# Kernel optimization log

Hardware: AMD Instinct MI355X
Metric: run time of the kernel (lower is better)

The kernel has to match this reference:

```python
import jax, jax.numpy as jnp
import numpy as np

N_NODES = 3000
N_FEAT = 2
N_UNITS = 64
BATCH = 16
K_DIFF = 2  # max_diffusion_step


def _supports(adj):
    # dual_random_walk: (D^-1 A)^T and (D'^-1 A^T)^T, rows with zero degree -> 0
    def rw_T(A):
        d = A.sum(axis=1)
        d_inv = jnp.where(d > 0, 1.0 / d, 0.0)
        return (d_inv[:, None] * A).T  # (N, N)
    return [rw_T(adj), rw_T(adj.T)]


def _gconv(inputs, state, supports, W, b, num_nodes):
    # inputs: (B, N*F), state: (B, N*U)
    B = inputs.shape[0]
    x = jnp.concatenate([inputs.reshape(B, num_nodes, -1),
                         state.reshape(B, num_nodes, -1)], axis=2)  # (B, N, C)
    x0 = x.transpose(1, 2, 0)  # (N, C, B)
    mats = [x0]
    for S in supports:
        x1 = jnp.einsum('mn,ncb->mcb', S, x0)
        mats.append(x1)
        xk_1, xk_2 = x1, x0
        for _ in range(2, K_DIFF + 1):
            x2 = 2.0 * jnp.einsum('mn,ncb->mcb', S, xk_1) - xk_2  # Chebyshev recurrence
            mats.append(x2)
            xk_1, xk_2 = x2, xk_1
    xs = jnp.stack(mats, axis=0)  # (M, N, C, B)
    M, _, C, _ = xs.shape
    xs = xs.transpose(3, 1, 2, 0).reshape(B * num_nodes, C * M)
    out = xs @ W + b  # (B*N, O)
    return out.reshape(B, num_nodes * W.shape[1])


def setup_inputs() -> dict:
    key = jax.random.key(0)
    k1, k2, k3, k4, k5 = jax.random.split(key, 5)
    C = N_FEAT + N_UNITS          # 66
    M = 2 * K_DIFF + 1            # 5 (two supports)
    xw = lambda k, s: jax.random.normal(k, s, dtype=jnp.float32) * jnp.sqrt(2.0 / (s[0] + s[1]))
    return {
        "inputs": jax.random.normal(k1, (BATCH, N_NODES * N_FEAT), dtype=jnp.float32),
        "hx": jax.random.normal(k2, (BATCH, N_NODES * N_UNITS), dtype=jnp.float32),
        "adj_mx": jax.random.uniform(k3, (N_NODES, N_NODES), dtype=jnp.float32),
        "W_gate": xw(k4, (C * M, 2 * N_UNITS)),
        "b_gate": jnp.ones((2 * N_UNITS,), dtype=jnp.float32),  # bias_start=1.0
        "W_cand": xw(k5, (C * M, N_UNITS)),
        "b_cand": jnp.zeros((N_UNITS,), dtype=jnp.float32),
        "num_nodes": N_NODES,
    }


def reference(inputs, hx, adj_mx, W_gate, b_gate, W_cand, b_cand, num_nodes):
    supports = _supports(adj_mx)
    B = inputs.shape[0]
    value = jax.nn.sigmoid(_gconv(inputs, hx, supports, W_gate, b_gate, num_nodes))
    value = value.reshape(B, num_nodes, 2 * N_UNITS)
    r, u = value[..., :N_UNITS], value[..., N_UNITS:]
    r = r.reshape(B, num_nodes * N_UNITS)
    u = u.reshape(B, num_nodes * N_UNITS)
    c = jnp.tanh(_gconv(inputs, r * hx, supports, W_cand, b_cand, num_nodes))
    new_state = u * hx + (1.0 - u) * c
    return new_state
```

## Files before the change

kernel.cpp:

```cpp
#include <hip/hip_runtime.h>
#include <cstdint>
#include <cstddef>


typedef unsigned short u16;
typedef __bf16 bf16x8 __attribute__((ext_vector_type(8)));
typedef u16 u16x8 __attribute__((ext_vector_type(8)));
typedef float f32x4 __attribute__((ext_vector_type(4)));

#define NND 3000
#define KP  3008
#define NBX 16
#define NCB 1056
#define NCBP 1152
#define KW  330
#define KWP 352

__device__ __forceinline__ float b2f(u16 x) { return (float)__builtin_bit_cast(__bf16, x); }
__device__ __forceinline__ u16 f2b(float f) { return __builtin_bit_cast(u16, (__bf16)f); }

__device__ __forceinline__ void gll16(const u16* g, void* l) {
  __builtin_amdgcn_global_load_lds(
      (const __attribute__((address_space(1))) unsigned int*)g,
      (__attribute__((address_space(3))) unsigned int*)l, 16, 0, 0);
}


__global__ void k_probe(const u16* __restrict__ bg, int* __restrict__ flag) {
  if (threadIdx.x == 0 && blockIdx.x == 0) *flag = (bg[0] == 0x3F80) ? 0 : 1;
}

__device__ __forceinline__ float rdf(const void* p, size_t i, int mode) {
  return mode ? ((const float*)p)[i] : b2f(((const u16*)p)[i]);
}


__global__ __launch_bounds__(256) void k_sums(const void* __restrict__ A,
                                              float* __restrict__ d0sum, float* __restrict__ d1sum,
                                              const int* __restrict__ flag) {
  __shared__ float ldsx[64 * 65];
  const int C = blockIdx.x * 64, R = blockIdx.y * 64, t = threadIdx.x;
  const int mode = *flag;
#pragma unroll
  for (int ph = 0; ph < 16; ++ph) {
    int idx = t + ph * 256;
    int r = idx >> 6, c = idx & 63;
    int rg = R + r, cg = C + c;
    ldsx[r * 65 + c] = (rg < NND && cg < NND) ? rdf(A, (size_t)rg * NND + cg, mode) : 0.f;
  }
  __syncthreads();
  if (t < 64) {
    int rg = R + t;
    if (rg < NND) {
      float s = 0.f;
#pragma unroll 8
      for (int c = 0; c < 64; ++c) s += ldsx[t * 65 + c];
      atomicAdd(&d0sum[rg], s);
    }
  } else if (t < 128) {
    int cg = C + (t - 64);
    if (cg < NND) {
      float s = 0.f;
#pragma unroll 8
      for (int r = 0; r < 64; ++r) s += ldsx[r * 65 + (t - 64)];
      atomicAdd(&d1sum[cg], s);
    }
  }
}

__global__ __launch_bounds__(256) void k_sboth(const void* __restrict__ A, const float* __restrict__ d0sum,
                                               const float* __restrict__ d1sum,
                                               u16* __restrict__ S0, u16* __restrict__ S1,
                                               const int* __restrict__ flag) {
  __shared__ float ldsx[64 * 65];
  __shared__ float inv1c[64];
  __shared__ float inv0r[64];
  const int C = blockIdx.x * 64, R = blockIdx.y * 64, t = threadIdx.x;
  const int mode = *flag;
  if (t < 64) {
    int cg = C + t;
    float ds = (cg < NND) ? d1sum[cg] : 0.f;
    inv1c[t] = ds > 0.f ? 1.f / ds : 0.f;
  } else if (t < 128) {
    int rg = R + (t - 64);
    float ds = (rg < NND) ? d0sum[rg] : 0.f;
    inv0r[t - 64] = ds > 0.f ? 1.f / ds : 0.f;
  }
#pragma unroll
  for (int ph = 0; ph < 16; ++ph) {
    int idx = t + ph * 256;
    int r = idx >> 6, c = idx & 63;
    int rg = R + r, cg = C + c;
    ldsx[r * 65 + c] = (rg < NND && cg < NND) ? rdf(A, (size_t)rg * NND + cg, mode) : 0.f;
  }
  __syncthreads();
#pragma unroll
  for (int ph = 0; ph < 16; ++ph) {
    int idx = t + ph * 256;
    int mr = idx >> 6, nc = idx & 63;
    int m1 = R + mr, n1 = C + nc;
    if (m1 < NND && n1 < KP)
      S1[(size_t)m1 * KP + n1] = f2b(ldsx[mr * 65 + nc] * inv1c[nc]);
    int m0_ = C + mr, n0_ = R + nc;
    if (m0_ < NND && n0_ < KP)
      S0[(size_t)m0_ * KP + n0_] = f2b(ldsx[nc * 65 + mr] * inv0r[nc]);
  }
}

__global__ __launch_bounds__(256) void k_wt2(const void* __restrict__ Wg, const void* __restrict__ Wc,
                                             u16* __restrict__ Wtg, u16* __restrict__ Wtc,
                                             const int* __restrict__ flag) {
  const int idx = blockIdx.x * 256 + threadIdx.x;
  const int mode = *flag;
  if (idx < 128 * KWP) {
    int o = idx / KWP, k = idx - o * KWP;
    float v = (k < KW) ? rdf(Wg, (size_t)k * 128 + o, mode) : 0.f;
    Wtg[idx] = f2b(v);
  } else if (idx < 192 * KWP) {
    int i2 = idx - 128 * KWP;
    int o = i2 / KWP, k = i2 - o * KWP;
    float v = (k < KW) ? rdf(Wc, (size_t)k * 64 + o, mode) : 0.f;
    Wtc[i2] = f2b(v);
  }
}

__global__ __launch_bounds__(256) void k_buildx(const void* __restrict__ inp, const void* __restrict__ hx,
                                                u16* __restrict__ xtg, u16* __restrict__ xtc,
                                                u16* __restrict__ chx, const int* __restrict__ flag) {
  __shared__ __align__(16) u16 hxl[128 * 72];
  const int nt = blockIdx.x, b = blockIdx.y;
  const int n0 = nt * 128, t = threadIdx.x;
  const int mode = *flag;
#pragma unroll
  for (int i = 0; i < 4; ++i) {
    int id = t + 256 * i;
    int nl = id >> 3, og = (id & 7) * 8;
    int ng = n0 + nl; if (ng > NND - 1) ng = NND - 1;
    const size_t base = (size_t)b * 192000 + (size_t)ng * 64 + og;
    u16x8 v;
    if (mode) {
      const float* h = (const float*)hx + base;
      f32x4 lo = *(const f32x4*)h, hi = *(const f32x4*)(h + 4);
      v[0] = f2b(lo[0]); v[1] = f2b(lo[1]); v[2] = f2b(lo[2]); v[3] = f2b(lo[3]);
      v[4] = f2b(hi[0]); v[5] = f2b(hi[1]); v[6] = f2b(hi[2]); v[7] = f2b(hi[3]);
    } else {
      v = *(const u16x8*)&((const u16*)hx)[base];
    }
    *(u16x8*)&hxl[nl * 72 + og] = v;
  }
  __syncthreads();
#pragma unroll
  for (int i = 0; i < 4; ++i) {
    int id = t + 256 * i;
    int nl = id >> 3, og = (id & 7) * 8;
    int ng = n0 + nl;
    if (ng < NND)
      *(u16x8*)&chx[(size_t)b * 192000 + (size_t)ng * 64 + og] = *(u16x8*)&hxl[nl * 72 + og];
  }
#pragma unroll
  for (int i = 0; i < 4; ++i) {
    int id = t + 256 * i;
    int u = id >> 4, ngrp = (id & 15) * 8;
    int nb = n0 + ngrp;
    if (nb < KP) {
      u16x8 v;
#pragma unroll
      for (int e = 0; e < 8; ++e) {
        int ng = nb + e;
        v[e] = (ng < NND) ? hxl[(ngrp + e) * 72 + u] : (u16)0;
      }
      *(u16x8*)&xtg[(size_t)((2 + u) * 16 + b) * KP + nb] = v;
    }
  }
  if (t < 32) {
    int c = t >> 4, ngrp = (t & 15) * 8;
    int nb = n0 + ngrp;
    if (nb < KP) {
      u16x8 v;
#pragma unroll
      for (int e = 0; e < 8; ++e) {
        int ng = nb + e;
        v[e] = (ng < NND) ? f2b(rdf(inp, (size_t)b * 6000 + (size_t)ng * 2 + c, mode)) : (u16)0;
      }
      *(u16x8*)&xtg[(size_t)(c * 16 + b) * KP + nb] = v;
      *(u16x8*)&xtc[(size_t)(c * 16 + b) * KP + nb] = v;
    }
  }
  if (nt == 23 && t < 64) {
    u16x8 z = {0, 0, 0, 0, 0, 0, 0, 0};
    *(u16x8*)&xtc[(size_t)((2 + t) * 16 + b) * KP + NND] = z;
  }
}

struct GemmAParams {
  const u16* A0; const u16* A1;
  const u16* B0; const u16* B1;
  u16* D0; u16* D1;
  const u16* X;
  int mode;
};

__global__ __launch_bounds__(256, 2) void k_gemmA(GemmAParams p) {
  __shared__ __align__(16) u16 lds[32768];
  const int bid = blockIdx.x;
  const int x8 = bid & 7, g = bid >> 3;
  const int slot = g / 9, n_idx = g - slot * 9;
  const int strip = x8 * 6 + slot;
  const int m_idx = strip >> 1, z = strip & 1;
  const u16* Sp = z ? p.A1 : p.A0;
  const u16* Bp = z ? p.B1 : p.B0;
  u16* Dp = z ? p.D1 : p.D0;
  const int n0 = n_idx * 128;
  const int m0 = m_idx * 128;
  const int t = threadIdx.x;
  const int lane = t & 63, w = t >> 6;
  const int wr = w >> 1, wc = w & 1;
  const int l15 = lane & 15, lq = lane >> 4;
  const int x7 = l15 & 7;

  const u16* gsrc[8];
  int lbase[8];
#pragma unroll
  for (int q = 0; q < 8; ++q) {
    const int c = t + 256 * q;
    if (c < 1024) {
      const int row = c >> 3, grp = c & 7;
      int mg = m0 + row; if (mg > NND - 1) mg = NND - 1;
      gsrc[q] = Sp + (size_t)mg * KP + ((grp ^ (row & 7)) << 3);
      lbase[q] = q * 4096 + w * 1024;
    } else {
      const int c2 = c - 1024;
      const int row = c2 >> 3, grp = c2 & 7;
      gsrc[q] = Bp + (size_t)(n0 + row) * KP + ((grp ^ (row & 7)) << 3);
      lbase[q] = 16384 + (q - 4) * 4096 + w * 1024;
    }
  }

  f32x4 acc[4][4];
#pragma unroll
  for (int i = 0; i < 4; ++i)
#pragma unroll
    for (int j = 0; j < 4; ++j) acc[i][j] = (f32x4){0.f, 0.f, 0.f, 0.f};

  auto STAGE = [&](int buf) {
    char* L = (char*)lds + buf * 32768;
#pragma unroll
    for (int q = 0; q < 8; ++q) { gll16(gsrc[q], (void*)(L + lbase[q])); gsrc[q] += 64; }
  };
  auto STEP = [&](int buf) {
    const u16* L = lds + buf * 16384;
    bf16x8 af[4][2], bf[4][2];
#pragma unroll
    for (int kk = 0; kk < 2; ++kk) {
#pragma unroll
      for (int i = 0; i < 4; ++i)
        af[i][kk] = *(const bf16x8*)&L[(wr * 64 + i * 16 + l15) * 64 + (((kk * 4 + lq) ^ x7) << 3)];
#pragma unroll
      for (int j = 0; j < 4; ++j)
        bf[j][kk] = *(const bf16x8*)&L[8192 + (wc * 64 + j * 16 + l15) * 64 + (((kk * 4 + lq) ^ x7) << 3)];
    }
#pragma unroll
    for (int kk = 0; kk < 2; ++kk)
#pragma unroll
      for (int i = 0; i < 4; ++i)
#pragma unroll
        for (int j = 0; j < 4; ++j)
          acc[i][j] = __builtin_amdgcn_mfma_f32_16x16x32_bf16(af[i][kk], bf[j][kk], acc[i][j], 0, 0, 0);
  };

  STAGE(0);
  for (int ks = 0; ks < 47; ++ks) {
    const int buf = ks & 1;
    if (ks < 46) {
      STAGE(buf ^ 1);
      asm volatile("s_waitcnt vmcnt(8)" ::: "memory");
    } else {
      asm volatile("s_waitcnt vmcnt(0)" ::: "memory");
    }
    __builtin_amdgcn_s_barrier();
    __builtin_amdgcn_sched_barrier(0);
    STEP(buf);
    __builtin_amdgcn_sched_barrier(0);
    __builtin_amdgcn_s_barrier();
  }

  __syncthreads();
  u16* Tw = &lds[w * 4608];
#pragma unroll
  for (int i = 0; i < 4; ++i)
#pragma unroll
    for (int j = 0; j < 4; ++j)
#pragma unroll
      for (int r = 0; r < 4; ++r) {
        int miw = i * 16 + lq * 4 + r;
        int niw = j * 16 + l15;
        float v = acc[i][j][r];
        if (m0 + wr * 64 + miw >= NND) v = 0.f;
        Tw[niw * 72 + miw] = f2b(v);
      }
  const int row8 = lane >> 3, colg = (lane & 7) * 8;
#pragma unroll
  for (int ph = 0; ph < 8; ++ph) {
    int nrow = ph * 8 + row8;
    int n_g = n0 + wc * 64 + nrow;
    int m_b = m0 + wr * 64 + colg;
    if (m_b < KP) {
      u16x8 y = *(u16x8*)&Tw[nrow * 72 + colg];
      if (p.mode) {
        const u16x8 x = *(const u16x8*)&p.X[(size_t)n_g * KP + m_b];
#pragma unroll
        for (int e = 0; e < 8; ++e) y[e] = f2b(2.f * b2f(y[e]) - b2f(x[e]));
      }
      *(u16x8*)&Dp[(size_t)n_g * KP + m_b] = y;
    }
  }
}

struct GateParams {
  const u16* xall;
  const u16* Wt;
  const void* bias;
  const u16* hx;
  u16* xtc;
  u16* ut;
  const int* flag;
};

__global__ __launch_bounds__(256, 2) void k_gate(GateParams p) {
  __shared__ __align__(16) u16 Al[128 * 40];
  __shared__ __align__(16) u16 Bl[64 * 40];
  __shared__ __align__(16) u16 hxl[64 * 72];
  __shared__ int rowA[KWP];
  const int b = blockIdx.y, n0 = blockIdx.x * 64;
  const int t = threadIdx.x, lane = t & 63, w = t >> 6, wr = w >> 1, wc = w & 1;
  const int l15 = lane & 15, lq = lane >> 4;
  const int mode = *p.flag;

  for (int k = t; k < KWP; k += 256) {
    int c = k / 5, mt = k - c * 5;
    rowA[k] = (k < KW) ? (mt * NCBP + c * 16 + b) * KP : 0;
  }
#pragma unroll
  for (int i = 0; i < 2; ++i) {
    int id = t + 256 * i;
    int nl = id >> 3, og = (id & 7) * 8;
    int ng = n0 + nl; if (ng > NND - 1) ng = NND - 1;
    *(u16x8*)&hxl[nl * 72 + og] = *(const u16x8*)&p.hx[(size_t)b * 192000 + (size_t)ng * 64 + og];
  }
  __syncthreads();

  f32x4 acc[4][2];
#pragma unroll
  for (int i = 0; i < 4; ++i)
#pragma unroll
    for (int j = 0; j < 2; ++j) acc[i][j] = (f32x4){0.f, 0.f, 0.f, 0.f};

  u16x8 aReg[2]; u16x8 bReg;
#pragma unroll
  for (int hh = 0; hh < 2; ++hh) {
    int id = t + 256 * hh;
    int r = id >> 2, g = id & 3;
    aReg[hh] = *(const u16x8*)&p.Wt[(size_t)r * KWP + g * 8];
  }
#pragma unroll
  for (int e = 0; e < 8; ++e) {
    int k = w * 8 + e;
    u16 x = p.xall[(size_t)rowA[k] + n0 + lane];
    bReg[e] = (k < KW) ? x : (u16)0;
  }

  for (int ks = 0; ks < 11; ++ks) {
    __syncthreads();
#pragma unroll
    for (int hh = 0; hh < 2; ++hh) {
      int id = t + 256 * hh;
      int r = id >> 2, g = id & 3;
      *(u16x8*)&Al[r * 40 + g * 8] = aReg[hh];
    }
    *(u16x8*)&Bl[lane * 40 + w * 8] = bReg;
    __syncthreads();

    if (ks + 1 < 11) {
      const int k0 = (ks + 1) * 32;
#pragma unroll
      for (int hh = 0; hh < 2; ++hh) {
        int id = t + 256 * hh;
        int r = id >> 2, g = id & 3;
        aReg[hh] = *(const u16x8*)&p.Wt[(size_t)r * KWP + k0 + g * 8];
      }
#pragma unroll
      for (int e = 0; e < 8; ++e) {
        int k = k0 + w * 8 + e;
        u16 x = p.xall[(size_t)rowA[k] + n0 + lane];
        bReg[e] = (k < KW) ? x : (u16)0;
      }
    }

    bf16x8 af[4], bf[2];
#pragma unroll
    for (int i = 0; i < 4; ++i) af[i] = *(const bf16x8*)&Al[(wr * 64 + i * 16 + l15) * 40 + lq * 8];
#pragma unroll
    for (int j = 0; j < 2; ++j) bf[j] = *(const bf16x8*)&Bl[(wc * 32 + j * 16 + l15) * 40 + lq * 8];
#pragma unroll
    for (int i = 0; i < 4; ++i)
#pragma unroll
      for (int j = 0; j < 2; ++j)
        acc[i][j] = __builtin_amdgcn_mfma_f32_16x16x32_bf16(af[i], bf[j], acc[i][j], 0, 0, 0);
  }

#pragma unroll
  for (int i = 0; i < 4; ++i)
#pragma unroll
    for (int j = 0; j < 2; ++j)
#pragma unroll
      for (int r = 0; r < 4; ++r) {
        int o = wr * 64 + i * 16 + lq * 4 + r;
        int nl = wc * 32 + j * 16 + l15;
        int ng = n0 + nl;
        if (ng < NND) {
          float v = acc[i][j][r] + rdf(p.bias, o, mode);
          float s = 1.f / (1.f + __expf(-v));
          if (o < 64) {
            float rh = s * b2f(hxl[nl * 72 + o]);
            p.xtc[(size_t)((o + 2) * 16 + b) * KP + ng] = f2b(rh);
          } else {
            p.ut[(size_t)b * 192000 + (size_t)(o - 64) * NND + ng] = f2b(s);
          }
        }
      }
}

struct CandParams {
  const u16* xall;
  const u16* Wt;
  const void* bias;
  const u16* hx;
  const u16* ut;
  void* out;
  const int* flag;
};

__global__ __launch_bounds__(256, 2) void k_cand(CandParams p) {
  __shared__ __align__(16) u16 Al[64 * 40];
  __shared__ __align__(16) u16 Bl[64 * 40];
  __shared__ __align__(16) u16 hxl[64 * 72];
  __shared__ __align__(16) u16 newl[64 * 72];
  __shared__ int rowA[KWP];
  const int b = blockIdx.y, n0 = blockIdx.x * 64;
  const int t = threadIdx.x, lane = t & 63, w = t >> 6, wr = w >> 1, wc = w & 1;
  const int l15 = lane & 15, lq = lane >> 4;
  const int mode = *p.flag;

  for (int k = t; k < KWP; k += 256) {
    int c = k / 5, mt = k - c * 5;
    rowA[k] = (k < KW) ? (mt * NCBP + c * 16 + b) * KP : 0;
  }
#pragma unroll
  for (int i = 0; i < 2; ++i) {
    int id = t + 256 * i;
    int nl = id >> 3, og = (id & 7) * 8;
    int ng = n0 + nl; if (ng > NND - 1) ng = NND - 1;
    *(u16x8*)&hxl[nl * 72 + og] = *(const u16x8*)&p.hx[(size_t)b * 192000 + (size_t)ng * 64 + og];
  }
  __syncthreads();

  f32x4 acc[2][2];
#pragma unroll
  for (int i = 0; i < 2; ++i)
#pragma unroll
    for (int j = 0; j < 2; ++j) acc[i][j] = (f32x4){0.f, 0.f, 0.f, 0.f};

  u16x8 aReg; u16x8 bReg;
  {
    int r = t >> 2, g = t & 3;
    aReg = *(const u16x8*)&p.Wt[(size_t)r * KWP + g * 8];
  }
#pragma unroll
  for (int e = 0; e < 8; ++e) {
    int k = w * 8 + e;
    u16 x = p.xall[(size_t)rowA[k] + n0 + lane];
    bReg[e] = (k < KW) ? x : (u16)0;
  }

  for (int ks = 0; ks < 11; ++ks) {
    __syncthreads();
    {
      int r = t >> 2, g = t & 3;
      *(u16x8*)&Al[r * 40 + g * 8] = aReg;
    }
    *(u16x8*)&Bl[lane * 40 + w * 8] = bReg;
    __syncthreads();

    if (ks + 1 < 11) {
      const int k0 = (ks + 1) * 32;
      {
        int r = t >> 2, g = t & 3;
        aReg = *(const u16x8*)&p.Wt[(size_t)r * KWP + k0 + g * 8];
      }
#pragma unroll
      for (int e = 0; e < 8; ++e) {
        int k = k0 + w * 8 + e;
        u16 x = p.xall[(size_t)rowA[k] + n0 + lane];
        bReg[e] = (k < KW) ? x : (u16)0;
      }
    }

    bf16x8 af[2], bf[2];
#pragma unroll
    for (int i = 0; i < 2; ++i) af[i] = *(const bf16x8*)&Al[(wr * 32 + i * 16 + l15) * 40 + lq * 8];
#pragma unroll
    for (int j = 0; j < 2; ++j) bf[j] = *(const bf16x8*)&Bl[(wc * 32 + j * 16 + l15) * 40 + lq * 8];
#pragma unroll
    for (int i = 0; i < 2; ++i)
#pragma unroll
      for (int j = 0; j < 2; ++j)
        acc[i][j] = __builtin_amdgcn_mfma_f32_16x16x32_bf16(af[i], bf[j], acc[i][j], 0, 0, 0);
  }

#pragma unroll
  for (int i = 0; i < 2; ++i)
#pragma unroll
    for (int j = 0; j < 2; ++j)
#pragma unroll
      for (int r = 0; r < 4; ++r) {
        int o = wr * 32 + i * 16 + lq * 4 + r;
        int nl = wc * 32 + j * 16 + l15;
        int ng = n0 + nl; int ngc = ng > NND - 1 ? NND - 1 : ng;
        float v = acc[i][j][r] + rdf(p.bias, o, mode);
        float c = tanhf(v);
        float u = b2f(p.ut[(size_t)b * 192000 + (size_t)o * NND + ngc]);
        float h = b2f(hxl[nl * 72 + o]);
        newl[nl * 72 + o] = f2b(u * h + (1.f - u) * c);
      }
  __syncthreads();
#pragma unroll
  for (int i = 0; i < 2; ++i) {
    int id = t + 256 * i;
    int nl = id >> 3, og = (id & 7) * 8;
    int ng = n0 + nl;
    if (ng < NND) {
      u16x8 v = *(u16x8*)&newl[nl * 72 + og];
      if (mode) {
        float* of = (float*)p.out + (size_t)b * 192000 + (size_t)ng * 64 + og;
        f32x4 lo = {b2f(v[0]), b2f(v[1]), b2f(v[2]), b2f(v[3])};
        f32x4 hi = {b2f(v[4]), b2f(v[5]), b2f(v[6]), b2f(v[7])};
        *(f32x4*)of = lo;
        *(f32x4*)(of + 4) = hi;
      } else {
        *(u16x8*)&((u16*)p.out)[(size_t)b * 192000 + (size_t)ng * 64 + og] = v;
      }
    }
  }
}


extern "C" void kernel_launch(void* const* d_in, const int* in_sizes, int n_in,
                              void* d_out, int out_size, void* d_ws, size_t ws_size,
                              hipStream_t stream) {
  const size_t SLP = (size_t)NCBP * KP;
  size_t off = 0;
  auto alloc = [&](size_t bytes) {
    void* pp = (char*)d_ws + off;
    off += (bytes + 255) & ~(size_t)255;
    return pp;
  };
  u16* S0  = (u16*)alloc((size_t)NND * KP * 2);
  u16* S1  = (u16*)alloc((size_t)NND * KP * 2);
  u16* Xg  = (u16*)alloc(5 * SLP * 2);
  u16* Xc  = (u16*)alloc(5 * SLP * 2);
  u16* Ut  = (u16*)alloc((size_t)NBX * 64 * NND * 2);
  u16* Wtg = (u16*)alloc((size_t)128 * KWP * 2);
  u16* Wtc = (u16*)alloc((size_t)64 * KWP * 2);
  float* dsums = (float*)alloc(2 * NND * 4);
  u16* cHx  = (u16*)alloc((size_t)3072000 * 2);
  int* flag = (int*)alloc(256);
  (void)in_sizes; (void)n_in; (void)out_size;

  if (ws_size < off) return;

  float* d0sum = dsums;
  float* d1sum = dsums + NND;

  u16* Xtg = Xg;            u16* Y1 = Xg + SLP;  u16* Z2 = Xg + 2 * SLP;
  u16* Y3 = Xg + 3 * SLP;   u16* Z4 = Xg + 4 * SLP;
  u16* Xtc = Xc;            u16* Y1c = Xc + SLP; u16* Z2c = Xc + 2 * SLP;
  u16* Y3c = Xc + 3 * SLP;  u16* Z4c = Xc + 4 * SLP;

  const void* inp = d_in[0];
  const void* hx  = d_in[1];
  const void* adj = d_in[2];
  const void* Wg  = d_in[3];
  const void* bg  = d_in[4];
  const void* Wc  = d_in[5];
  const void* bc  = d_in[6];

  k_probe<<<1, 64, 0, stream>>>((const u16*)bg, flag);
  hipMemsetAsync(dsums, 0, 2 * NND * 4, stream);
  k_sums<<<dim3(47, 47), 256, 0, stream>>>(adj, d0sum, d1sum, flag);
  k_sboth<<<dim3(47, 47), 256, 0, stream>>>(adj, d0sum, d1sum, S0, S1, flag);
  k_wt2<<<264, 256, 0, stream>>>(Wg, Wc, Wtg, Wtc, flag);
  k_buildx<<<dim3(24, NBX), 256, 0, stream>>>(inp, hx, Xtg, Xtc, cHx, flag);

  GemmAParams g1 = {S0, S1, Xtg, Xtg, Y1, Y3, nullptr, 0};
  k_gemmA<<<432, 256, 0, stream>>>(g1);
  GemmAParams g2 = {S0, S1, Y1, Y3, Z2, Z4, Xtg, 1};
  k_gemmA<<<432, 256, 0, stream>>>(g2);

  GateParams gp = {Xg, Wtg, bg, cHx, Xtc, Ut, flag};
  k_gate<<<dim3(47, NBX), 256, 0, stream>>>(gp);

  GemmAParams g3 = {S0, S1, Xtc, Xtc, Y1c, Y3c, nullptr, 0};
  k_gemmA<<<432, 256, 0, stream>>>(g3);
  GemmAParams g4 = {S0, S1, Y1c, Y3c, Z2c, Z4c, Xtc, 1};
  k_gemmA<<<432, 256, 0, stream>>>(g4);

  CandParams cp = {Xc, Wtc, bc, cHx, Ut, d_out, flag};
  k_cand<<<dim3(47, NBX), 256, 0, stream>>>(cp);
}
```

Measured before the change: 371.4 us.

## Fuse prep kernels into one launch and enlarge diffusion GEMM tiles to 256x128

The probe, row/column-sum, weight-transpose and input-build kernels are merged into one multi-role k_prep launch. Every kernel now derives the dtype mode inline from the bias instead of reading a flag buffer. Row sums are computed per row with a wave reduction instead of tiled atomics. The diffusion GEMM moves from 128x128 tiles with 256 threads and 2 blocks per CU to 256x128 tiles with 512 threads and 1 block per CU, halving the grid to 216 blocks. This cuts launch overhead and reloads of the shared operand, but leaves fewer blocks than CUs, uses more LDS per block and gives less latency hiding.

```diff
diff --git a/kernel.cpp b/kernel.cpp
--- a/kernel.cpp
+++ b/kernel.cpp
@@ -19,51 +19,143 @@
 __device__ __forceinline__ float b2f(u16 x) { return (float)__builtin_bit_cast(__bf16, x); }
 __device__ __forceinline__ u16 f2b(float f) { return __builtin_bit_cast(u16, (__bf16)f); }
 
+__device__ __forceinline__ int getmode(const u16* bgp) { return (bgp[0] == 0x3F80) ? 0 : 1; }
+
+__device__ __forceinline__ float rdf(const void* p, size_t i, int mode) {
+  return mode ? ((const float*)p)[i] : b2f(((const u16*)p)[i]);
+}
+
 __device__ __forceinline__ void gll16(const u16* g, void* l) {
   __builtin_amdgcn_global_load_lds(
       (const __attribute__((address_space(1))) unsigned int*)g,
       (__attribute__((address_space(3))) unsigned int*)l, 16, 0, 0);
 }
 
-
-__global__ void k_probe(const u16* __restrict__ bg, int* __restrict__ flag) {
-  if (threadIdx.x == 0 && blockIdx.x == 0) *flag = (bg[0] == 0x3F80) ? 0 : 1;
-}
-
-__device__ __forceinline__ float rdf(const void* p, size_t i, int mode) {
-  return mode ? ((const float*)p)[i] : b2f(((const u16*)p)[i]);
-}
-
-
-__global__ __launch_bounds__(256) void k_sums(const void* __restrict__ A,
-                                              float* __restrict__ d0sum, float* __restrict__ d1sum,
-                                              const int* __restrict__ flag) {
-  __shared__ float ldsx[64 * 65];
-  const int C = blockIdx.x * 64, R = blockIdx.y * 64, t = threadIdx.x;
-  const int mode = *flag;
-#pragma unroll
-  for (int ph = 0; ph < 16; ++ph) {
-    int idx = t + ph * 256;
-    int r = idx >> 6, c = idx & 63;
-    int rg = R + r, cg = C + c;
-    ldsx[r * 65 + c] = (rg < NND && cg < NND) ? rdf(A, (size_t)rg * NND + cg, mode) : 0.f;
-  }
-  __syncthreads();
-  if (t < 64) {
-    int rg = R + t;
-    if (rg < NND) {
-      float s = 0.f;
-#pragma unroll 8
-      for (int c = 0; c < 64; ++c) s += ldsx[t * 65 + c];
-      atomicAdd(&d0sum[rg], s);
-    }
-  } else if (t < 128) {
-    int cg = C + (t - 64);
-    if (cg < NND) {
-      float s = 0.f;
-#pragma unroll 8
-      for (int r = 0; r < 64; ++r) s += ldsx[r * 65 + (t - 64)];
-      atomicAdd(&d1sum[cg], s);
+struct PrepParams {
+  const void* A;
+  const void* Wg; const void* Wc;
+  const void* inp; const void* hx;
+  const u16* bgp;
+  float* d0sum; float* d1sum;
+  u16* Wtg; u16* Wtc;
+  u16* xtg; u16* xtc; u16* chx;
+};
+
+__global__ __launch_bounds__(256) void k_prep(PrepParams p) {
+  const int bid = blockIdx.x, t = threadIdx.x;
+  const int mode = getmode(p.bgp);
+
+  if (bid < 3000) {
+    const int row = bid;
+    float s = 0.f;
+    if (mode) {
+      const float* a = (const float*)p.A + (size_t)row * NND;
+      for (int j = t; j < NND; j += 256) s += a[j];
+    } else {
+      const u16* a = (const u16*)p.A + (size_t)row * NND;
+      for (int j = t; j < NND; j += 256) s += b2f(a[j]);
+    }
+    for (int off = 32; off; off >>= 1) s += __shfl_down(s, off, 64);
+    __shared__ float red[4];
+    if ((t & 63) == 0) red[t >> 6] = s;
+    __syncthreads();
+    if (t == 0) p.d0sum[row] = red[0] + red[1] + red[2] + red[3];
+    return;
+  }
+  if (bid < 3360) {
+    const int idx = bid - 3000;
+    const int cs = idx % 12, rs = idx / 12;
+    const int j = cs * 256 + t;
+    if (j >= NND) return;
+    const int i0 = rs * 100;
+    float s = 0.f;
+    if (mode) {
+      const float* a = (const float*)p.A;
+      for (int i = i0; i < i0 + 100; ++i) s += a[(size_t)i * NND + j];
+    } else {
+      const u16* a = (const u16*)p.A;
+      for (int i = i0; i < i0 + 100; ++i) s += b2f(a[(size_t)i * NND + j]);
+    }
+    atomicAdd(&p.d1sum[j], s);
+    return;
+  }
+  if (bid < 3624) {
+    const int idx = (bid - 3360) * 256 + t;
+    if (idx < 128 * KWP) {
+      int o = idx / KWP, k = idx - o * KWP;
+      float v = (k < KW) ? rdf(p.Wg, (size_t)k * 128 + o, mode) : 0.f;
+      p.Wtg[idx] = f2b(v);
+    } else if (idx < 192 * KWP) {
+      int i2 = idx - 128 * KWP;
+      int o = i2 / KWP, k = i2 - o * KWP;
+      float v = (k < KW) ? rdf(p.Wc, (size_t)k * 64 + o, mode) : 0.f;
+      p.Wtc[i2] = f2b(v);
+    }
+    return;
+  }
+  {
+    const int idx = bid - 3624;
+    const int nt = idx % 24, b = idx / 24;
+    const int n0 = nt * 128;
+    __shared__ __align__(16) u16 hxl[128 * 72];
+#pragma unroll
+    for (int i = 0; i < 4; ++i) {
+      int id = t + 256 * i;
+      int nl = id >> 3, og = (id & 7) * 8;
+      int ng = n0 + nl; if (ng > NND - 1) ng = NND - 1;
+      const size_t base = (size_t)b * 192000 + (size_t)ng * 64 + og;
+      u16x8 v;
+      if (mode) {
+        const float* h = (const float*)p.hx + base;
+        f32x4 lo = *(const f32x4*)h, hi = *(const f32x4*)(h + 4);
+        v[0] = f2b(lo[0]); v[1] = f2b(lo[1]); v[2] = f2b(lo[2]); v[3] = f2b(lo[3]);
+        v[4] = f2b(hi[0]); v[5] = f2b(hi[1]); v[6] = f2b(hi[2]); v[7] = f2b(hi[3]);
+      } else {
+        v = *(const u16x8*)&((const u16*)p.hx)[base];
+      }
+      *(u16x8*)&hxl[nl * 72 + og] = v;
+    }
+    __syncthreads();
+#pragma unroll
+    for (int i = 0; i < 4; ++i) {
+      int id = t + 256 * i;
+      int nl = id >> 3, og = (id & 7) * 8;
+      int ng = n0 + nl;
+      if (ng < NND)
+        *(u16x8*)&p.chx[(size_t)b * 192000 + (size_t)ng * 64 + og] = *(u16x8*)&hxl[nl * 72 + og];
+    }
+#pragma unroll
+    for (int i = 0; i < 4; ++i) {
+      int id = t + 256 * i;
+      int u = id >> 4, ngrp = (id & 15) * 8;
+      int nb = n0 + ngrp;
+      if (nb < KP) {
+        u16x8 v;
+#pragma unroll
+        for (int e = 0; e < 8; ++e) {
+          int ng = nb + e;
+          v[e] = (ng < NND) ? hxl[(ngrp + e) * 72 + u] : (u16)0;
+        }
+        *(u16x8*)&p.xtg[(size_t)((2 + u) * 16 + b) * KP + nb] = v;
+      }
+    }
+    if (t < 32) {
+      int c = t >> 4, ngrp = (t & 15) * 8;
+      int nb = n0 + ngrp;
+      if (nb < KP) {
+        u16x8 v;
+#pragma unroll
+        for (int e = 0; e < 8; ++e) {
+          int ng = nb + e;
+          v[e] = (ng < NND) ? f2b(rdf(p.inp, (size_t)b * 6000 + (size_t)ng * 2 + c, mode)) : (u16)0;
+        }
+        *(u16x8*)&p.xtg[(size_t)(c * 16 + b) * KP + nb] = v;
+        *(u16x8*)&p.xtc[(size_t)(c * 16 + b) * KP + nb] = v;
+      }
+    }
+    if (nt == 23 && t < 64) {
+      u16x8 z = {0, 0, 0, 0, 0, 0, 0, 0};
+      *(u16x8*)&p.xtc[(size_t)((2 + t) * 16 + b) * KP + NND] = z;
     }
   }
 }
@@ -71,12 +163,12 @@
 __global__ __launch_bounds__(256) void k_sboth(const void* __restrict__ A, const float* __restrict__ d0sum,
                                                const float* __restrict__ d1sum,
                                                u16* __restrict__ S0, u16* __restrict__ S1,
-                                               const int* __restrict__ flag) {
+                                               const u16* __restrict__ bgp) {
   __shared__ float ldsx[64 * 65];
   __shared__ float inv1c[64];
   __shared__ float inv0r[64];
   const int C = blockIdx.x * 64, R = blockIdx.y * 64, t = threadIdx.x;
-  const int mode = *flag;
+  const int mode = getmode(bgp);
   if (t < 64) {
     int cg = C + t;
     float ds = (cg < NND) ? d1sum[cg] : 0.f;
@@ -107,91 +199,6 @@
   }
 }
 
-__global__ __launch_bounds__(256) void k_wt2(const void* __restrict__ Wg, const void* __restrict__ Wc,
-                                             u16* __restrict__ Wtg, u16* __restrict__ Wtc,
-                                             const int* __restrict__ flag) {
-  const int idx = blockIdx.x * 256 + threadIdx.x;
-  const int mode = *flag;
-  if (idx < 128 * KWP) {
-    int o = idx / KWP, k = idx - o * KWP;
-    float v = (k < KW) ? rdf(Wg, (size_t)k * 128 + o, mode) : 0.f;
-    Wtg[idx] = f2b(v);
-  } else if (idx < 192 * KWP) {
-    int i2 = idx - 128 * KWP;
-    int o = i2 / KWP, k = i2 - o * KWP;
-    float v = (k < KW) ? rdf(Wc, (size_t)k * 64 + o, mode) : 0.f;
-    Wtc[i2] = f2b(v);
-  }
-}
-
-__global__ __launch_bounds__(256) void k_buildx(const void* __restrict__ inp, const void* __restrict__ hx,
-                                                u16* __restrict__ xtg, u16* __restrict__ xtc,
-                                                u16* __restrict__ chx, const int* __restrict__ flag) {
-  __shared__ __align__(16) u16 hxl[128 * 72];
-  const int nt = blockIdx.x, b = blockIdx.y;
-  const int n0 = nt * 128, t = threadIdx.x;
-  const int mode = *flag;
-#pragma unroll
-  for (int i = 0; i < 4; ++i) {
-    int id = t + 256 * i;
-    int nl = id >> 3, og = (id & 7) * 8;
-    int ng = n0 + nl; if (ng > NND - 1) ng = NND - 1;
-    const size_t base = (size_t)b * 192000 + (size_t)ng * 64 + og;
-    u16x8 v;
-    if (mode) {
-      const float* h = (const float*)hx + base;
-      f32x4 lo = *(const f32x4*)h, hi = *(const f32x4*)(h + 4);
-      v[0] = f2b(lo[0]); v[1] = f2b(lo[1]); v[2] = f2b(lo[2]); v[3] = f2b(lo[3]);
-      v[4] = f2b(hi[0]); v[5] = f2b(hi[1]); v[6] = f2b(hi[2]); v[7] = f2b(hi[3]);
-    } else {
-      v = *(const u16x8*)&((const u16*)hx)[base];
-    }
-    *(u16x8*)&hxl[nl * 72 + og] = v;
-  }
-  __syncthreads();
-#pragma unroll
-  for (int i = 0; i < 4; ++i) {
-    int id = t + 256 * i;
-    int nl = id >> 3, og = (id & 7) * 8;
-    int ng = n0 + nl;
-    if (ng < NND)
-      *(u16x8*)&chx[(size_t)b * 192000 + (size_t)ng * 64 + og] = *(u16x8*)&hxl[nl * 72 + og];
-  }
-#pragma unroll
-  for (int i = 0; i < 4; ++i) {
-    int id = t + 256 * i;
-    int u = id >> 4, ngrp = (id & 15) * 8;
-    int nb = n0 + ngrp;
-    if (nb < KP) {
-      u16x8 v;
-#pragma unroll
-      for (int e = 0; e < 8; ++e) {
-        int ng = nb + e;
-        v[e] = (ng < NND) ? hxl[(ngrp + e) * 72 + u] : (u16)0;
-      }
-      *(u16x8*)&xtg[(size_t)((2 + u) * 16 + b) * KP + nb] = v;
-    }
-  }
-  if (t < 32) {
-    int c = t >> 4, ngrp = (t & 15) * 8;
-    int nb = n0 + ngrp;
-    if (nb < KP) {
-      u16x8 v;
-#pragma unroll
-      for (int e = 0; e < 8; ++e) {
-        int ng = nb + e;
-        v[e] = (ng < NND) ? f2b(rdf(inp, (size_t)b * 6000 + (size_t)ng * 2 + c, mode)) : (u16)0;
-      }
-      *(u16x8*)&xtg[(size_t)(c * 16 + b) * KP + nb] = v;
-      *(u16x8*)&xtc[(size_t)(c * 16 + b) * KP + nb] = v;
-    }
-  }
-  if (nt == 23 && t < 64) {
-    u16x8 z = {0, 0, 0, 0, 0, 0, 0, 0};
-    *(u16x8*)&xtc[(size_t)((2 + t) * 16 + b) * KP + NND] = z;
-  }
-}
-
 struct GemmAParams {
   const u16* A0; const u16* A1;
   const u16* B0; const u16* B1;
@@ -200,39 +207,39 @@
   int mode;
 };
 
-__global__ __launch_bounds__(256, 2) void k_gemmA(GemmAParams p) {
-  __shared__ __align__(16) u16 lds[32768];
+__global__ __launch_bounds__(512, 1) void k_gemmA(GemmAParams p) {
+  __shared__ __align__(16) u16 lds[49152];
   const int bid = blockIdx.x;
   const int x8 = bid & 7, g = bid >> 3;
-  const int slot = g / 9, n_idx = g - slot * 9;
-  const int strip = x8 * 6 + slot;
+  const int gs = g / 9, n_idx = g - gs * 9;
+  const int strip = x8 * 3 + gs;
   const int m_idx = strip >> 1, z = strip & 1;
   const u16* Sp = z ? p.A1 : p.A0;
   const u16* Bp = z ? p.B1 : p.B0;
   u16* Dp = z ? p.D1 : p.D0;
   const int n0 = n_idx * 128;
-  const int m0 = m_idx * 128;
+  const int m0 = m_idx * 256;
   const int t = threadIdx.x;
   const int lane = t & 63, w = t >> 6;
   const int wr = w >> 1, wc = w & 1;
   const int l15 = lane & 15, lq = lane >> 4;
   const int x7 = l15 & 7;
 
-  const u16* gsrc[8];
-  int lbase[8];
-#pragma unroll
-  for (int q = 0; q < 8; ++q) {
-    const int c = t + 256 * q;
-    if (c < 1024) {
+  const u16* gsrc[6];
+  int lbase[6];
+#pragma unroll
+  for (int q = 0; q < 6; ++q) {
+    const int c = t + 512 * q;
+    if (c < 2048) {
       const int row = c >> 3, grp = c & 7;
       int mg = m0 + row; if (mg > NND - 1) mg = NND - 1;
       gsrc[q] = Sp + (size_t)mg * KP + ((grp ^ (row & 7)) << 3);
-      lbase[q] = q * 4096 + w * 1024;
+      lbase[q] = q * 8192 + w * 1024;
     } else {
-      const int c2 = c - 1024;
+      const int c2 = c - 2048;
       const int row = c2 >> 3, grp = c2 & 7;
       gsrc[q] = Bp + (size_t)(n0 + row) * KP + ((grp ^ (row & 7)) << 3);
-      lbase[q] = 16384 + (q - 4) * 4096 + w * 1024;
+      lbase[q] = 32768 + (q - 4) * 8192 + w * 1024;
     }
   }
 
@@ -243,12 +250,12 @@
     for (int j = 0; j < 4; ++j) acc[i][j] = (f32x4){0.f, 0.f, 0.f, 0.f};
 
   auto STAGE = [&](int buf) {
-    char* L = (char*)lds + buf * 32768;
-#pragma unroll
-    for (int q = 0; q < 8; ++q) { gll16(gsrc[q], (void*)(L + lbase[q])); gsrc[q] += 64; }
+    char* L = (char*)lds + buf * 49152;
+#pragma unroll
+    for (int q = 0; q < 6; ++q) { gll16(gsrc[q], (void*)(L + lbase[q])); gsrc[q] += 64; }
   };
   auto STEP = [&](int buf) {
-    const u16* L = lds + buf * 16384;
+    const u16* L = lds + buf * 24576;
     bf16x8 af[4][2], bf[4][2];
 #pragma unroll
     for (int kk = 0; kk < 2; ++kk) {
@@ -257,7 +264,7 @@
         af[i][kk] = *(const bf16x8*)&L[(wr * 64 + i * 16 + l15) * 64 + (((kk * 4 + lq) ^ x7) << 3)];
 #pragma unroll
       for (int j = 0; j < 4; ++j)
-        bf[j][kk] = *(const bf16x8*)&L[8192 + (wc * 64 + j * 16 + l15) * 64 + (((kk * 4 + lq) ^ x7) << 3)];
+        bf[j][kk] = *(const bf16x8*)&L[16384 + (wc * 64 + j * 16 + l15) * 64 + (((kk * 4 + lq) ^ x7) << 3)];
     }
 #pragma unroll
     for (int kk = 0; kk < 2; ++kk)
@@ -273,7 +280,7 @@
     const int buf = ks & 1;
     if (ks < 46) {
       STAGE(buf ^ 1);
-      asm volatile("s_waitcnt vmcnt(8)" ::: "memory");
+      asm volatile("s_waitcnt vmcnt(6)" ::: "memory");
     } else {
       asm volatile("s_waitcnt vmcnt(0)" ::: "memory");
     }
@@ -323,7 +330,7 @@
   const u16* hx;
   u16* xtc;
   u16* ut;
-  const int* flag;
+  const u16* bgp;
 };
 
 __global__ __launch_bounds__(256, 2) void k_gate(GateParams p) {
@@ -334,7 +341,7 @@
   const int b = blockIdx.y, n0 = blockIdx.x * 64;
   const int t = threadIdx.x, lane = t & 63, w = t >> 6, wr = w >> 1, wc = w & 1;
   const int l15 = lane & 15, lq = lane >> 4;
-  const int mode = *p.flag;
+  const int mode = getmode(p.bgp);
 
   for (int k = t; k < KWP; k += 256) {
     int c = k / 5, mt = k - c * 5;
@@ -437,7 +444,7 @@
   const u16* hx;
   const u16* ut;
   void* out;
-  const int* flag;
+  const u16* bgp;
 };
 
 __global__ __launch_bounds__(256, 2) void k_cand(CandParams p) {
@@ -449,7 +456,7 @@
   const int b = blockIdx.y, n0 = blockIdx.x * 64;
   const int t = threadIdx.x, lane = t & 63, w = t >> 6, wr = w >> 1, wc = w & 1;
   const int l15 = lane & 15, lq = lane >> 4;
-  const int mode = *p.flag;
+  const int mode = getmode(p.bgp);
 
   for (int k = t; k < KWP; k += 256) {
     int c = k / 5, mt = k - c * 5;
@@ -573,7 +580,6 @@
   u16* Wtc = (u16*)alloc((size_t)64 * KWP * 2);
   float* dsums = (float*)alloc(2 * NND * 4);
   u16* cHx  = (u16*)alloc((size_t)3072000 * 2);
-  int* flag = (int*)alloc(256);
   (void)in_sizes; (void)n_in; (void)out_size;
 
   if (ws_size < off) return;
@@ -590,30 +596,28 @@
   const void* hx  = d_in[1];
   const void* adj = d_in[2];
   const void* Wg  = d_in[3];
-  const void* bg  = d_in[4];
+  const u16*  bg  = (const u16*)d_in[4];
   const void* Wc  = d_in[5];
   const void* bc  = d_in[6];
 
-  k_probe<<<1, 64, 0, stream>>>((const u16*)bg, flag);
   hipMemsetAsync(dsums, 0, 2 * NND * 4, stream);
-  k_sums<<<dim3(47, 47), 256, 0, stream>>>(adj, d0sum, d1sum, flag);
-  k_sboth<<<dim3(47, 47), 256, 0, stream>>>(adj, d0sum, d1sum, S0, S1, flag);
-  k_wt2<<<264, 256, 0, stream>>>(Wg, Wc, Wtg, Wtc, flag);
-  k_buildx<<<dim3(24, NBX), 256, 0, stream>>>(inp, hx, Xtg, Xtc, cHx, flag);
+  PrepParams pp = {adj, Wg, Wc, inp, hx, bg, d0sum, d1sum, Wtg, Wtc, Xtg, Xtc, cHx};
+  k_prep<<<4008, 256, 0, stream>>>(pp);
+  k_sboth<<<dim3(47, 47), 256, 0, stream>>>(adj, d0sum, d1sum, S0, S1, bg);
 
   GemmAParams g1 = {S0, S1, Xtg, Xtg, Y1, Y3, nullptr, 0};
-  k_gemmA<<<432, 256, 0, stream>>>(g1);
+  k_gemmA<<<216, 512, 0, stream>>>(g1);
   GemmAParams g2 = {S0, S1, Y1, Y3, Z2, Z4, Xtg, 1};
-  k_gemmA<<<432, 256, 0, stream>>>(g2);
-
-  GateParams gp = {Xg, Wtg, bg, cHx, Xtc, Ut, flag};
+  k_gemmA<<<216, 512, 0, stream>>>(g2);
+
+  GateParams gp = {Xg, Wtg, bg, cHx, Xtc, Ut, bg};
   k_gate<<<dim3(47, NBX), 256, 0, stream>>>(gp);
 
   GemmAParams g3 = {S0, S1, Xtc, Xtc, Y1c, Y3c, nullptr, 0};
-  k_gemmA<<<432, 256, 0, stream>>>(g3);
+  k_gemmA<<<216, 512, 0, stream>>>(g3);
   GemmAParams g4 = {S0, S1, Y1c, Y3c, Z2c, Z4c, Xtc, 1};
-  k_gemmA<<<432, 256, 0, stream>>>(g4);
-
-  CandParams cp = {Xc, Wtc, bc, cHx, Ut, d_out, flag};
+  k_gemmA<<<216, 512, 0, stream>>>(g4);
+
+  CandParams cp = {Xc, Wtc, bc, cHx, Ut, d_out, bg};
   k_cand<<<dim3(47, NBX), 256, 0, stream>>>(cp);
 }
```

Measured after the change: 381.2 us. 2.6% more time.
